# Optimization experiments

Measured on AMD Instinct MI355X. Metric: run time of the kernel, lower is better.

## Reference

```python
import jax, jax.numpy as jnp
import numpy as np

B, L, H, HD, NK, NQ = 2, 1024, 2048, 64, 4, 32
NPREV = NQ - NK  # 28 KV heads gathered from previous layers


def _rotate_half(x):
    x1, x2 = jnp.split(x, 2, axis=-1)
    return jnp.concatenate((-x2, x1), axis=-1)


def _apply_rope(cos, sin, x):
    length = x.shape[-2]
    return x * cos[..., -length:, :] + _rotate_half(x) * sin[..., -length:, :]


def setup_inputs() -> dict:
    key = jax.random.key(0)
    ks = jax.random.split(key, 7)
    hidden_states = jax.random.normal(ks[0], (B, L, H), jnp.float32)
    prev_k = jax.random.normal(ks[1], (B, NPREV, L, HD), jnp.float32)
    prev_v = jax.random.normal(ks[2], (B, NPREV, L, HD), jnp.float32)
    s = 0.02
    Wq = jax.random.normal(ks[3], (NQ * HD, H), jnp.float32) * s
    Wk = jax.random.normal(ks[4], (NK * HD, H), jnp.float32) * s
    Wv = jax.random.normal(ks[5], (NK * HD, H), jnp.float32) * s
    Wo = jax.random.normal(ks[6], (H, NQ * HD), jnp.float32) * s
    # RoPE tables (duplicated-half layout matching rotate_half)
    inv_freq = 1.0 / (10000.0 ** (jnp.arange(0, HD, 2, dtype=jnp.float32) / HD))
    freqs = jnp.arange(L, dtype=jnp.float32)[:, None] * inv_freq[None, :]
    emb = jnp.concatenate((freqs, freqs), axis=-1)  # [L, HD]
    cos = jnp.cos(emb)[None, None]  # [1,1,L,HD]
    sin = jnp.sin(emb)[None, None]
    attention_mask = jnp.tril(jnp.ones((L, L), dtype=bool))[None, None]  # [1,1,L,L]
    return {"hidden_states": hidden_states, "prev_k": prev_k, "prev_v": prev_v,
            "Wq": Wq, "Wk": Wk, "Wv": Wv, "Wo": Wo,
            "cos": cos, "sin": sin, "attention_mask": attention_mask}


def reference(hidden_states, prev_k, prev_v, Wq, Wk, Wv, Wo, cos, sin, attention_mask):
    Bv, Lv, _ = hidden_states.shape
    # QKV projections (torch Linear: x @ W.T)
    q = (hidden_states @ Wq.T).reshape(Bv, Lv, NQ, HD).transpose(0, 2, 1, 3)  # [B,NQ,L,HD]
    k_new = (hidden_states @ Wk.T).reshape(Bv, Lv, NK, HD).transpose(0, 2, 1, 3)
    v_new = (hidden_states @ Wv.T).reshape(Bv, Lv, NK, HD).transpose(0, 2, 1, 3)
    # DeCAN cross-layer cache update: stack previous layers' KV heads + current
    k = jnp.concatenate((prev_k, k_new), axis=1)  # [B,NQ,L,HD]
    v = jnp.concatenate((prev_v, v_new), axis=1)
    # RoPE after cache gather (same positions for all stacked layers)
    q = _apply_rope(cos, sin, q)
    k = _apply_rope(cos, sin, k)
    # SDPA with additive log-mask (log(bool) == 0 / -inf; broadcast == repeat)
    add_mask = jnp.where(attention_mask, jnp.float32(0.0), jnp.float32(-1e30))
    scores = jnp.einsum('bhqd,bhkd->bhqk', q, k) * (HD ** -0.5) + add_mask
    attn = jax.nn.softmax(scores, axis=-1)
    out = jnp.einsum('bhqk,bhkd->bhqd', attn, v)  # [B,NQ,L,HD]
    out = out.transpose(0, 2, 1, 3).reshape(Bv, Lv, NQ * HD)
    return out @ Wo.T  # [B,L,H]
```

## Files before the change

### kernel.cpp

```cpp
#include <hip/hip_runtime.h>
#include <stdint.h>

#define L_SEQ 1024
#define NHEAD 32
#define NPREV 28
#define HDIM  64
#define HID   2048
#define NPROJ 2560

typedef __bf16 bf16_t;
typedef bf16_t bf16x8 __attribute__((ext_vector_type(8)));
typedef float  f32x4  __attribute__((ext_vector_type(4)));

__device__ __forceinline__ ushort f2bf(float x) {
    union { float f; uint32_t u; } v; v.f = x;
    uint32_t r = v.u + 0x7fffu + ((v.u >> 16) & 1u);
    return (ushort)(r >> 16);
}
__device__ __forceinline__ ushort f2bf_t(float x) {
    union { float f; uint32_t u; } v; v.f = x;
    return (ushort)(v.u >> 16);
}
__device__ __forceinline__ float bf2f(ushort u) {
    union { uint32_t u; float f; } v; v.u = ((uint32_t)u) << 16; return v.f;
}
__device__ __forceinline__ void cvt8(float* dst, uint4 u) {
    union { uint32_t u; float f; } t;
    t.u = u.x << 16;         dst[0] = t.f;
    t.u = u.x & 0xffff0000u; dst[1] = t.f;
    t.u = u.y << 16;         dst[2] = t.f;
    t.u = u.y & 0xffff0000u; dst[3] = t.f;
    t.u = u.z << 16;         dst[4] = t.f;
    t.u = u.z & 0xffff0000u; dst[5] = t.f;
    t.u = u.w << 16;         dst[6] = t.f;
    t.u = u.w & 0xffff0000u; dst[7] = t.f;
}

#define GLB(p) ((const __attribute__((address_space(1))) void*)(p))
#define LDS(p) ((__attribute__((address_space(3))) void*)(p))

__global__ void cvt_all(const float* __restrict__ s0, const float* __restrict__ s1,
                        const float* __restrict__ s2, const float* __restrict__ s3,
                        const float* __restrict__ s4,
                        ushort* __restrict__ d0, ushort* __restrict__ d1,
                        ushort* __restrict__ d2, ushort* __restrict__ d3,
                        ushort* __restrict__ d4) {
    int blk = blockIdx.x;
    const float* src; ushort* dst; int idx;
    if      (blk < 4096) { src = s0; dst = d0; idx = blk; }
    else if (blk < 8192) { src = s1; dst = d1; idx = blk - 4096; }
    else if (blk < 8704) { src = s2; dst = d2; idx = blk - 8192; }
    else if (blk < 9216) { src = s3; dst = d3; idx = blk - 8704; }
    else                 { src = s4; dst = d4; idx = blk - 9216; }
    int i = idx * 256 + threadIdx.x;
    float4 v = ((const float4*)src)[i];
    ushort4 o;
    o.x = f2bf(v.x); o.y = f2bf(v.y); o.z = f2bf(v.z); o.w = f2bf(v.w);
    ((ushort4*)dst)[i] = o;
}

__global__ __launch_bounds__(256, 3) void gemm_bt(const ushort* __restrict__ A,
                                                  const ushort* __restrict__ B,
                                                  ushort* __restrict__ C0,
                                                  ushort* __restrict__ C1,
                                                  int M, int N, int K) {
    __shared__ __align__(16) ushort Ash[2 * 4096];
    __shared__ __align__(16) ushort Bsh[2 * 8192];
    const int tid  = threadIdx.x;
    const int lane = tid & 63;
    const int wave = tid >> 6;
    const int quad = lane >> 4;
    const int l16  = lane & 15;
    const int m0 = blockIdx.y * 64;
    const int n0 = blockIdx.x * 128;
    const int wm = (wave >> 1) * 32;
    const int wn = (wave & 1) * 64;
    const int kb = blockIdx.z * (K >> 1);
    const int ke = kb + (K >> 1);
    ushort* C = blockIdx.z ? C1 : C0;

    f32x4 acc[2][4] = {};

    const int sb = ((tid & 3) ^ ((tid >> 3) & 3)) * 8;
    const ushort* Ag = A + (long)(m0 + (tid >> 2)) * K + sb;
    const ushort* Bg = B + (long)(n0 + (tid >> 2)) * K + sb;
    const int woff = wave * 512;
    const int swz = (quad ^ ((l16 >> 1) & 3)) * 8;

    __builtin_amdgcn_global_load_lds(GLB(Ag + kb),                LDS(Ash + woff),               16, 0, 0);
    __builtin_amdgcn_global_load_lds(GLB(Ag + kb + 32),           LDS(Ash + 2048 + woff),        16, 0, 0);
    __builtin_amdgcn_global_load_lds(GLB(Bg + kb),                LDS(Bsh + woff),               16, 0, 0);
    __builtin_amdgcn_global_load_lds(GLB(Bg + 64L * K + kb),      LDS(Bsh + 2048 + woff),        16, 0, 0);
    __builtin_amdgcn_global_load_lds(GLB(Bg + kb + 32),           LDS(Bsh + 4096 + woff),        16, 0, 0);
    __builtin_amdgcn_global_load_lds(GLB(Bg + 64L * K + kb + 32), LDS(Bsh + 4096 + 2048 + woff), 16, 0, 0);

    int cur = 0;
    for (int k0 = kb; k0 < ke; k0 += 64) {
        __syncthreads();
        if (k0 + 64 < ke) {
            const int na = (cur ^ 1) * 4096;
            const int nb = (cur ^ 1) * 8192;
            const ushort* Agn = Ag + k0 + 64;
            const ushort* Bgn = Bg + k0 + 64;
            __builtin_amdgcn_global_load_lds(GLB(Agn),                LDS(Ash + na + woff),               16, 0, 0);
            __builtin_amdgcn_global_load_lds(GLB(Agn + 32),           LDS(Ash + na + 2048 + woff),        16, 0, 0);
            __builtin_amdgcn_global_load_lds(GLB(Bgn),                LDS(Bsh + nb + woff),               16, 0, 0);
            __builtin_amdgcn_global_load_lds(GLB(Bgn + 64L * K),      LDS(Bsh + nb + 2048 + woff),        16, 0, 0);
            __builtin_amdgcn_global_load_lds(GLB(Bgn + 32),           LDS(Bsh + nb + 4096 + woff),        16, 0, 0);
            __builtin_amdgcn_global_load_lds(GLB(Bgn + 64L * K + 32), LDS(Bsh + nb + 4096 + 2048 + woff), 16, 0, 0);
        }
        const ushort* As = Ash + cur * 4096;
        const ushort* Bs = Bsh + cur * 8192;
#pragma unroll
        for (int h = 0; h < 2; h++) {
            bf16x8 af[2], bf[4];
#pragma unroll
            for (int i = 0; i < 2; i++)
                af[i] = *(const bf16x8*)(As + h * 2048 + (wm + i * 16 + l16) * 32 + swz);
#pragma unroll
            for (int i = 0; i < 4; i++)
                bf[i] = *(const bf16x8*)(Bs + h * 4096 + (wn + i * 16 + l16) * 32 + swz);
#pragma unroll
            for (int mi = 0; mi < 2; mi++)
#pragma unroll
                for (int ni = 0; ni < 4; ni++)
                    acc[mi][ni] = __builtin_amdgcn_mfma_f32_16x16x32_bf16(af[mi], bf[ni], acc[mi][ni], 0, 0, 0);
        }
        cur ^= 1;
    }
#pragma unroll
    for (int mi = 0; mi < 2; mi++)
#pragma unroll
        for (int ni = 0; ni < 4; ni++)
#pragma unroll
            for (int r = 0; r < 4; r++) {
                int m = m0 + wm + mi * 16 + quad * 4 + r;
                int n = n0 + wn + ni * 16 + l16;
                C[(long)m * N + n] = f2bf(acc[mi][ni][r]);
            }
}

__global__ void add2(const ushort* __restrict__ a, const ushort* __restrict__ b,
                     float* __restrict__ out) {
    int i = blockIdx.x * 256 + threadIdx.x;
    uint4 ua = ((const uint4*)a)[i];
    uint4 ub = ((const uint4*)b)[i];
    float fa[8], fb[8];
    cvt8(fa, ua); cvt8(fb, ub);
    float4 o0 = {fa[0] + fb[0], fa[1] + fb[1], fa[2] + fb[2], fa[3] + fb[3]};
    float4 o1 = {fa[4] + fb[4], fa[5] + fb[5], fa[6] + fb[6], fa[7] + fb[7]};
    ((float4*)out)[2 * i]     = o0;
    ((float4*)out)[2 * i + 1] = o1;
}

__global__ __launch_bounds__(256) void prep_qkv(const ushort* __restrict__ pa,
                                                const ushort* __restrict__ pb,
                                                const float* __restrict__ prev_k,
                                                const float* __restrict__ prev_v,
                                                const float* __restrict__ cosb,
                                                const float* __restrict__ sinb,
                                                ushort* __restrict__ Qr,
                                                ushort* __restrict__ Kr,
                                                ushort* __restrict__ Vt) {
    __shared__ __align__(16) ushort T[64 * 72];
    const int t  = threadIdx.x;
    const int l0 = blockIdx.x * 64;
    const int bh = blockIdx.y;
    const int b  = bh >> 5, h = bh & 31;
    const int r  = t >> 2;
    const int c0 = (t & 3) * 8;
    const int l  = l0 + r;
    const long prow = ((long)(b * L_SEQ + l)) * NPROJ;
    const long base = (long)bh * (L_SEQ * HDIM);

    float cv[8], sv[8];
    *(float4*)(cv)     = *(const float4*)(cosb + l * 64 + c0);
    *(float4*)(cv + 4) = *(const float4*)(cosb + l * 64 + c0 + 4);
    *(float4*)(sv)     = *(const float4*)(sinb + l * 64 + c0);
    *(float4*)(sv + 4) = *(const float4*)(sinb + l * 64 + c0 + 4);

    const float SC = 0.125f * 1.44269504f;

    {
        float xl[8], xh[8], yl[8], yh[8];
        cvt8(xl, *(const uint4*)(pa + prow + h * 64 + c0));
        cvt8(xh, *(const uint4*)(pa + prow + h * 64 + c0 + 32));
        cvt8(yl, *(const uint4*)(pb + prow + h * 64 + c0));
        cvt8(yh, *(const uint4*)(pb + prow + h * 64 + c0 + 32));
        ushort ol[8], oh[8];
#pragma unroll
        for (int i = 0; i < 8; i++) {
            float a = xl[i] + yl[i], c = xh[i] + yh[i];
            ol[i] = f2bf((a * cv[i] - c * sv[i]) * SC);
            oh[i] = f2bf((c * cv[i] + a * sv[i]) * SC);
        }
        ushort* q = Qr + base + (long)l * 64;
        *(uint4*)(q + c0)      = *(uint4*)ol;
        *(uint4*)(q + c0 + 32) = *(uint4*)oh;
    }
    {
        float xl[8], xh[8];
        if (h < NPREV) {
            const float* pk = prev_k + (((long)b * NPREV + h) * L_SEQ + l) * 64;
            *(float4*)(xl)     = *(const float4*)(pk + c0);
            *(float4*)(xl + 4) = *(const float4*)(pk + c0 + 4);
            *(float4*)(xh)     = *(const float4*)(pk + c0 + 32);
            *(float4*)(xh + 4) = *(const float4*)(pk + c0 + 36);
        } else {
            float yl[8], yh[8];
            cvt8(xl, *(const uint4*)(pa + prow + HID + (h - NPREV) * 64 + c0));
            cvt8(xh, *(const uint4*)(pa + prow + HID + (h - NPREV) * 64 + c0 + 32));
            cvt8(yl, *(const uint4*)(pb + prow + HID + (h - NPREV) * 64 + c0));
            cvt8(yh, *(const uint4*)(pb + prow + HID + (h - NPREV) * 64 + c0 + 32));
#pragma unroll
            for (int i = 0; i < 8; i++) { xl[i] += yl[i]; xh[i] += yh[i]; }
        }
        ushort ol[8], oh[8];
#pragma unroll
        for (int i = 0; i < 8; i++) {
            ol[i] = f2bf(xl[i] * cv[i] - xh[i] * sv[i]);
            oh[i] = f2bf(xh[i] * cv[i] + xl[i] * sv[i]);
        }
        ushort* k = Kr + base + (long)l * 64;
        *(uint4*)(k + c0)      = *(uint4*)ol;
        *(uint4*)(k + c0 + 32) = *(uint4*)oh;
    }
    {
        float xl[8], xh[8];
        if (h < NPREV) {
            const float* pv = prev_v + (((long)b * NPREV + h) * L_SEQ + l) * 64;
            *(float4*)(xl)     = *(const float4*)(pv + c0);
            *(float4*)(xl + 4) = *(const float4*)(pv + c0 + 4);
            *(float4*)(xh)     = *(const float4*)(pv + c0 + 32);
            *(float4*)(xh + 4) = *(const float4*)(pv + c0 + 36);
        } else {
            float yl[8], yh[8];
            cvt8(xl, *(const uint4*)(pa + prow + HID + 256 + (h - NPREV) * 64 + c0));
            cvt8(xh, *(const uint4*)(pa + prow + HID + 256 + (h - NPREV) * 64 + c0 + 32));
            cvt8(yl, *(const uint4*)(pb + prow + HID + 256 + (h - NPREV) * 64 + c0));
            cvt8(yh, *(const uint4*)(pb + prow + HID + 256 + (h - NPREV) * 64 + c0 + 32));
#pragma unroll
            for (int i = 0; i < 8; i++) { xl[i] += yl[i]; xh[i] += yh[i]; }
        }
#pragma unroll
        for (int i = 0; i < 8; i++) {
            T[(c0 + i) * 72 + r]      = f2bf(xl[i]);
            T[(c0 + 32 + i) * 72 + r] = f2bf(xh[i]);
        }
    }
    __syncthreads();
    {
        const int lc = (t & 3) * 16;
        uint4 o0 = *(const uint4*)(T + r * 72 + lc);
        uint4 o1 = *(const uint4*)(T + r * 72 + lc + 8);
        ushort* og = Vt + base + (long)r * L_SEQ + l0 + lc;
        *(uint4*)og       = o0;
        *(uint4*)(og + 8) = o1;
    }
}

#define KP 68
__global__ __launch_bounds__(256, 4) void attn_mfma(const ushort* __restrict__ Qr,
                                                    const ushort* __restrict__ Kr,
                                                    const ushort* __restrict__ Vt,
                                                    ushort* __restrict__ Oa) {
    __shared__ __align__(16) ushort Ksh[64 * KP];
    __shared__ __align__(16) ushort Vsh[64 * KP];
    __shared__ __align__(16) ushort Psh[4][16 * KP];

    const int tid  = threadIdx.x;
    const int lane = tid & 63;
    const int wave = tid >> 6;
    const int quad = lane >> 4;
    const int l16  = lane & 15;
    const int bh   = blockIdx.x;
    const int q0   = (15 - (int)blockIdx.y) * 64;
    const long base = (long)bh * (L_SEQ * HDIM);

    bf16x8 qf0, qf1;
    {
        const ushort* qp = Qr + base + (long)(q0 + wave * 16 + l16) * HDIM + quad * 8;
        qf0 = *(const bf16x8*)qp;
        qf1 = *(const bf16x8*)(qp + 32);
    }
    float lr[4] = {};
    f32x4 o[4] = {};

    const int srow  = tid >> 2;
    const int scol  = (tid & 3) * 16;
    const int row_l = wave * 16 + quad * 4;

    uint4 ka, kb, va, vb;
    {
        const ushort* kg = Kr + base + (long)srow * HDIM + scol;
        ka = *(const uint4*)kg; kb = *(const uint4*)(kg + 8);
        const ushort* vg = Vt + base + (long)srow * L_SEQ + scol;
        va = *(const uint4*)vg; vb = *(const uint4*)(vg + 8);
    }

    for (int kv0 = 0; kv0 <= q0; kv0 += 64) {
        __syncthreads();
        *(uint4*)(Ksh + srow * KP + scol)     = ka;
        *(uint4*)(Ksh + srow * KP + scol + 8) = kb;
        *(uint4*)(Vsh + srow * KP + scol)     = va;
        *(uint4*)(Vsh + srow * KP + scol + 8) = vb;
        __syncthreads();
        if (kv0 + 64 <= q0) {
            const ushort* kg = Kr + base + (long)(kv0 + 64 + srow) * HDIM + scol;
            ka = *(const uint4*)kg; kb = *(const uint4*)(kg + 8);
            const ushort* vg = Vt + base + (long)srow * L_SEQ + kv0 + 64 + scol;
            va = *(const uint4*)vg; vb = *(const uint4*)(vg + 8);
        }

        f32x4 s[4] = {};
#pragma unroll
        for (int nt = 0; nt < 4; nt++) {
            bf16x8 kf0 = *(const bf16x8*)(Ksh + (nt * 16 + l16) * KP + quad * 8);
            bf16x8 kf1 = *(const bf16x8*)(Ksh + (nt * 16 + l16) * KP + 32 + quad * 8);
            s[nt] = __builtin_amdgcn_mfma_f32_16x16x32_bf16(qf0, kf0, s[nt], 0, 0, 0);
            s[nt] = __builtin_amdgcn_mfma_f32_16x16x32_bf16(qf1, kf1, s[nt], 0, 0, 0);
        }

        const bool diag = (kv0 == q0);
#pragma unroll
        for (int nt = 0; nt < 4; nt++) {
            const int col = nt * 16 + l16;
#pragma unroll
            for (int r = 0; r < 4; r++) {
                float p = __builtin_exp2f(s[nt][r]);
                if (diag && col > row_l + r) p = 0.f;
                lr[r] += p;
                Psh[wave][(quad * 4 + r) * KP + col] = f2bf_t(p);
            }
        }

#pragma unroll
        for (int ks = 0; ks < 2; ks++) {
            bf16x8 pf = *(const bf16x8*)(&Psh[wave][l16 * KP + ks * 32 + quad * 8]);
#pragma unroll
            for (int nt = 0; nt < 4; nt++) {
                bf16x8 vf = *(const bf16x8*)(Vsh + (nt * 16 + l16) * KP + ks * 32 + quad * 8);
                o[nt] = __builtin_amdgcn_mfma_f32_16x16x32_bf16(pf, vf, o[nt], 0, 0, 0);
            }
        }
    }

    const int b = bh >> 5, h = bh & 31;
#pragma unroll
    for (int r = 0; r < 4; r++) {
        float a = lr[r];
        a += __shfl_xor(a, 1); a += __shfl_xor(a, 2); a += __shfl_xor(a, 4); a += __shfl_xor(a, 8);
        float inv = 1.f / a;
        long orow = (long)(b * L_SEQ + q0 + wave * 16 + quad * 4 + r) * HID + h * 64;
#pragma unroll
        for (int nt = 0; nt < 4; nt++)
            Oa[orow + nt * 16 + l16] = f2bf(o[nt][r] * inv);
    }
}

extern "C" void kernel_launch(void* const* d_in, const int* in_sizes, int n_in,
                              void* d_out, int out_size, void* d_ws, size_t ws_size,
                              hipStream_t stream) {
    const float* hs     = (const float*)d_in[0];
    const float* prev_k = (const float*)d_in[1];
    const float* prev_v = (const float*)d_in[2];
    const float* Wq     = (const float*)d_in[3];
    const float* Wk     = (const float*)d_in[4];
    const float* Wv     = (const float*)d_in[5];
    const float* Wo     = (const float*)d_in[6];
    const float* cosb   = (const float*)d_in[7];
    const float* sinb   = (const float*)d_in[8];
    float* out = (float*)d_out;

    ushort* hs_bf   = (ushort*)d_ws;
    ushort* wqkv_bf = hs_bf + 2048L * 2048;
    ushort* wo_bf   = wqkv_bf + 2560L * 2048;
    ushort* proj    = wo_bf + 2048L * 2048;
    ushort* Qr      = proj + 2048L * 2560;
    ushort* Kr      = Qr + 4194304;
    ushort* Vt      = Kr + 4194304;
    ushort* Oa      = Vt + 4194304;

    ushort* proj_b;
    if (ws_size >= (35651584UL + 5242880UL) * 2)
        proj_b = Oa + 4194304;
    else
        proj_b = (ushort*)(void*)d_in[0];

    ushort* outp_a = proj;
    ushort* outp_b = Qr;

    cvt_all<<<13312, 256, 0, stream>>>(hs, Wq, Wk, Wv, Wo,
                                       hs_bf, wqkv_bf,
                                       wqkv_bf + 2048L * 2048,
                                       wqkv_bf + 2304L * 2048,
                                       wo_bf);
    gemm_bt<<<dim3(20, 32, 2), 256, 0, stream>>>(hs_bf, wqkv_bf, proj, proj_b, 2048, 2560, 2048);
    prep_qkv<<<dim3(16, 64), 256, 0, stream>>>(proj, proj_b, prev_k, prev_v, cosb, sinb, Qr, Kr, Vt);
    attn_mfma<<<dim3(64, 16), 256, 0, stream>>>(Qr, Kr, Vt, Oa);
    gemm_bt<<<dim3(16, 32, 2), 256, 0, stream>>>(Oa, wo_bf, outp_a, outp_b, 2048, 2048, 2048);
    add2<<<2048, 256, 0, stream>>>(outp_a, outp_b, out);
}
```

Measured before the change: 237.5 us.

## Fuse prev-KV RoPE prep into QKV GEMM launch; single-pass fp32 output GEMM

The QKV projection GEMM grid now carries extra blocks that process the 28 previous-layer KV heads (RoPE on K, transpose of V). These blocks have no dependency on the GEMM, so that work can overlap with the matmul instead of running in a later kernel. The later prep kernel now handles only Q and the 4 new KV heads. The output projection drops split-K: it runs the full K range in one pass and writes fp32 directly, which removes the bf16 partial buffers and the add2 kernel. The costs are fewer blocks in the output GEMM (512 instead of 1024), which may leave the GPU less occupied, and a mixed-role kernel whose long GEMM blocks and short prep blocks can finish unevenly.

```diff
diff --git a/kernel.cpp b/kernel.cpp
--- a/kernel.cpp
+++ b/kernel.cpp
@@ -59,104 +59,154 @@
     ((ushort4*)dst)[i] = o;
 }
 
-__global__ __launch_bounds__(256, 3) void gemm_bt(const ushort* __restrict__ A,
-                                                  const ushort* __restrict__ B,
-                                                  ushort* __restrict__ C0,
-                                                  ushort* __restrict__ C1,
-                                                  int M, int N, int K) {
+__global__ __launch_bounds__(256, 3) void gemm1_fused(
+        const ushort* __restrict__ A, const ushort* __restrict__ B,
+        ushort* __restrict__ C0, ushort* __restrict__ C1,
+        const float* __restrict__ prev_k, const float* __restrict__ prev_v,
+        const float* __restrict__ cosb, const float* __restrict__ sinb,
+        ushort* __restrict__ Kr, ushort* __restrict__ Vt) {
     __shared__ __align__(16) ushort Ash[2 * 4096];
     __shared__ __align__(16) ushort Bsh[2 * 8192];
-    const int tid  = threadIdx.x;
-    const int lane = tid & 63;
-    const int wave = tid >> 6;
-    const int quad = lane >> 4;
-    const int l16  = lane & 15;
-    const int m0 = blockIdx.y * 64;
-    const int n0 = blockIdx.x * 128;
-    const int wm = (wave >> 1) * 32;
-    const int wn = (wave & 1) * 64;
-    const int kb = blockIdx.z * (K >> 1);
-    const int ke = kb + (K >> 1);
-    ushort* C = blockIdx.z ? C1 : C0;
-
-    f32x4 acc[2][4] = {};
-
-    const int sb = ((tid & 3) ^ ((tid >> 3) & 3)) * 8;
-    const ushort* Ag = A + (long)(m0 + (tid >> 2)) * K + sb;
-    const ushort* Bg = B + (long)(n0 + (tid >> 2)) * K + sb;
-    const int woff = wave * 512;
-    const int swz = (quad ^ ((l16 >> 1) & 3)) * 8;
-
-    __builtin_amdgcn_global_load_lds(GLB(Ag + kb),                LDS(Ash + woff),               16, 0, 0);
-    __builtin_amdgcn_global_load_lds(GLB(Ag + kb + 32),           LDS(Ash + 2048 + woff),        16, 0, 0);
-    __builtin_amdgcn_global_load_lds(GLB(Bg + kb),                LDS(Bsh + woff),               16, 0, 0);
-    __builtin_amdgcn_global_load_lds(GLB(Bg + 64L * K + kb),      LDS(Bsh + 2048 + woff),        16, 0, 0);
-    __builtin_amdgcn_global_load_lds(GLB(Bg + kb + 32),           LDS(Bsh + 4096 + woff),        16, 0, 0);
-    __builtin_amdgcn_global_load_lds(GLB(Bg + 64L * K + kb + 32), LDS(Bsh + 4096 + 2048 + woff), 16, 0, 0);
-
-    int cur = 0;
-    for (int k0 = kb; k0 < ke; k0 += 64) {
-        __syncthreads();
-        if (k0 + 64 < ke) {
-            const int na = (cur ^ 1) * 4096;
-            const int nb = (cur ^ 1) * 8192;
-            const ushort* Agn = Ag + k0 + 64;
-            const ushort* Bgn = Bg + k0 + 64;
-            __builtin_amdgcn_global_load_lds(GLB(Agn),                LDS(Ash + na + woff),               16, 0, 0);
-            __builtin_amdgcn_global_load_lds(GLB(Agn + 32),           LDS(Ash + na + 2048 + woff),        16, 0, 0);
-            __builtin_amdgcn_global_load_lds(GLB(Bgn),                LDS(Bsh + nb + woff),               16, 0, 0);
-            __builtin_amdgcn_global_load_lds(GLB(Bgn + 64L * K),      LDS(Bsh + nb + 2048 + woff),        16, 0, 0);
-            __builtin_amdgcn_global_load_lds(GLB(Bgn + 32),           LDS(Bsh + nb + 4096 + woff),        16, 0, 0);
-            __builtin_amdgcn_global_load_lds(GLB(Bgn + 64L * K + 32), LDS(Bsh + nb + 4096 + 2048 + woff), 16, 0, 0);
-        }
-        const ushort* As = Ash + cur * 4096;
-        const ushort* Bs = Bsh + cur * 8192;
-#pragma unroll
-        for (int h = 0; h < 2; h++) {
-            bf16x8 af[2], bf[4];
-#pragma unroll
-            for (int i = 0; i < 2; i++)
-                af[i] = *(const bf16x8*)(As + h * 2048 + (wm + i * 16 + l16) * 32 + swz);
-#pragma unroll
-            for (int i = 0; i < 4; i++)
-                bf[i] = *(const bf16x8*)(Bs + h * 4096 + (wn + i * 16 + l16) * 32 + swz);
-#pragma unroll
-            for (int mi = 0; mi < 2; mi++)
-#pragma unroll
-                for (int ni = 0; ni < 4; ni++)
-                    acc[mi][ni] = __builtin_amdgcn_mfma_f32_16x16x32_bf16(af[mi], bf[ni], acc[mi][ni], 0, 0, 0);
-        }
-        cur ^= 1;
-    }
-#pragma unroll
-    for (int mi = 0; mi < 2; mi++)
-#pragma unroll
-        for (int ni = 0; ni < 4; ni++)
-#pragma unroll
-            for (int r = 0; r < 4; r++) {
-                int m = m0 + wm + mi * 16 + quad * 4 + r;
-                int n = n0 + wn + ni * 16 + l16;
-                C[(long)m * N + n] = f2bf(acc[mi][ni][r]);
-            }
-}
-
-__global__ void add2(const ushort* __restrict__ a, const ushort* __restrict__ b,
-                     float* __restrict__ out) {
-    int i = blockIdx.x * 256 + threadIdx.x;
-    uint4 ua = ((const uint4*)a)[i];
-    uint4 ub = ((const uint4*)b)[i];
-    float fa[8], fb[8];
-    cvt8(fa, ua); cvt8(fb, ub);
-    float4 o0 = {fa[0] + fb[0], fa[1] + fb[1], fa[2] + fb[2], fa[3] + fb[3]};
-    float4 o1 = {fa[4] + fb[4], fa[5] + fb[5], fa[6] + fb[6], fa[7] + fb[7]};
-    ((float4*)out)[2 * i]     = o0;
-    ((float4*)out)[2 * i + 1] = o1;
-}
-
-__global__ __launch_bounds__(256) void prep_qkv(const ushort* __restrict__ pa,
+    const int g   = blockIdx.x;
+    const int tid = threadIdx.x;
+
+    if (g < 1280) {
+        const int K = 2048, N = NPROJ;
+        const int lane = tid & 63;
+        const int wave = tid >> 6;
+        const int quad = lane >> 4;
+        const int l16  = lane & 15;
+        const int z  = g / 640;
+        const int rb = g % 640;
+        const int n0 = (rb % 20) * 128;
+        const int m0 = (rb / 20) * 64;
+        const int wm = (wave >> 1) * 32;
+        const int wn = (wave & 1) * 64;
+        const int kb = z * 1024;
+        const int ke = kb + 1024;
+        ushort* C = z ? C1 : C0;
+
+        f32x4 acc[2][4] = {};
+
+        const int sb = ((tid & 3) ^ ((tid >> 3) & 3)) * 8;
+        const ushort* Ag = A + (long)(m0 + (tid >> 2)) * K + sb;
+        const ushort* Bg = B + (long)(n0 + (tid >> 2)) * K + sb;
+        const int woff = wave * 512;
+        const int swz = (quad ^ ((l16 >> 1) & 3)) * 8;
+
+        __builtin_amdgcn_global_load_lds(GLB(Ag + kb),                LDS(Ash + woff),               16, 0, 0);
+        __builtin_amdgcn_global_load_lds(GLB(Ag + kb + 32),           LDS(Ash + 2048 + woff),        16, 0, 0);
+        __builtin_amdgcn_global_load_lds(GLB(Bg + kb),                LDS(Bsh + woff),               16, 0, 0);
+        __builtin_amdgcn_global_load_lds(GLB(Bg + 64L * K + kb),      LDS(Bsh + 2048 + woff),        16, 0, 0);
+        __builtin_amdgcn_global_load_lds(GLB(Bg + kb + 32),           LDS(Bsh + 4096 + woff),        16, 0, 0);
+        __builtin_amdgcn_global_load_lds(GLB(Bg + 64L * K + kb + 32), LDS(Bsh + 4096 + 2048 + woff), 16, 0, 0);
+
+        int cur = 0;
+        for (int k0 = kb; k0 < ke; k0 += 64) {
+            __syncthreads();
+            if (k0 + 64 < ke) {
+                const int na = (cur ^ 1) * 4096;
+                const int nb = (cur ^ 1) * 8192;
+                const ushort* Agn = Ag + k0 + 64;
+                const ushort* Bgn = Bg + k0 + 64;
+                __builtin_amdgcn_global_load_lds(GLB(Agn),                LDS(Ash + na + woff),               16, 0, 0);
+                __builtin_amdgcn_global_load_lds(GLB(Agn + 32),           LDS(Ash + na + 2048 + woff),        16, 0, 0);
+                __builtin_amdgcn_global_load_lds(GLB(Bgn),                LDS(Bsh + nb + woff),               16, 0, 0);
+                __builtin_amdgcn_global_load_lds(GLB(Bgn + 64L * K),      LDS(Bsh + nb + 2048 + woff),        16, 0, 0);
+                __builtin_amdgcn_global_load_lds(GLB(Bgn + 32),           LDS(Bsh + nb + 4096 + woff),        16, 0, 0);
+                __builtin_amdgcn_global_load_lds(GLB(Bgn + 64L * K + 32), LDS(Bsh + nb + 4096 + 2048 + woff), 16, 0, 0);
+            }
+            const ushort* As = Ash + cur * 4096;
+            const ushort* Bs = Bsh + cur * 8192;
+#pragma unroll
+            for (int h = 0; h < 2; h++) {
+                bf16x8 af[2], bf[4];
+#pragma unroll
+                for (int i = 0; i < 2; i++)
+                    af[i] = *(const bf16x8*)(As + h * 2048 + (wm + i * 16 + l16) * 32 + swz);
+#pragma unroll
+                for (int i = 0; i < 4; i++)
+                    bf[i] = *(const bf16x8*)(Bs + h * 4096 + (wn + i * 16 + l16) * 32 + swz);
+#pragma unroll
+                for (int mi = 0; mi < 2; mi++)
+#pragma unroll
+                    for (int ni = 0; ni < 4; ni++)
+                        acc[mi][ni] = __builtin_amdgcn_mfma_f32_16x16x32_bf16(af[mi], bf[ni], acc[mi][ni], 0, 0, 0);
+            }
+            cur ^= 1;
+        }
+#pragma unroll
+        for (int mi = 0; mi < 2; mi++)
+#pragma unroll
+            for (int ni = 0; ni < 4; ni++)
+#pragma unroll
+                for (int r = 0; r < 4; r++) {
+                    int m = m0 + wm + mi * 16 + quad * 4 + r;
+                    int n = n0 + wn + ni * 16 + l16;
+                    C[(long)m * N + n] = f2bf(acc[mi][ni][r]);
+                }
+    } else {
+        const int idx = g - 1280;
+        const int lt  = idx & 15;
+        const int ph  = idx >> 4;
+        const int b   = ph / NPREV;
+        const int h   = ph % NPREV;
+        const int l0  = lt * 64;
+        const int r   = tid >> 2;
+        const int c0  = (tid & 3) * 8;
+        const int l   = l0 + r;
+        const int bh  = b * NHEAD + h;
+        const long base = (long)bh * (L_SEQ * HDIM);
+
+        float cv[8], sv[8];
+        *(float4*)(cv)     = *(const float4*)(cosb + l * 64 + c0);
+        *(float4*)(cv + 4) = *(const float4*)(cosb + l * 64 + c0 + 4);
+        *(float4*)(sv)     = *(const float4*)(sinb + l * 64 + c0);
+        *(float4*)(sv + 4) = *(const float4*)(sinb + l * 64 + c0 + 4);
+
+        {
+            const float* pk = prev_k + (((long)b * NPREV + h) * L_SEQ + l) * 64;
+            float xl[8], xh[8];
+            *(float4*)(xl)     = *(const float4*)(pk + c0);
+            *(float4*)(xl + 4) = *(const float4*)(pk + c0 + 4);
+            *(float4*)(xh)     = *(const float4*)(pk + c0 + 32);
+            *(float4*)(xh + 4) = *(const float4*)(pk + c0 + 36);
+            ushort ol[8], oh[8];
+#pragma unroll
+            for (int i = 0; i < 8; i++) {
+                ol[i] = f2bf(xl[i] * cv[i] - xh[i] * sv[i]);
+                oh[i] = f2bf(xh[i] * cv[i] + xl[i] * sv[i]);
+            }
+            ushort* k = Kr + base + (long)l * 64;
+            *(uint4*)(k + c0)      = *(uint4*)ol;
+            *(uint4*)(k + c0 + 32) = *(uint4*)oh;
+        }
+        {
+            ushort* T = Ash;
+            const float* pv = prev_v + (((long)b * NPREV + h) * L_SEQ + l) * 64;
+            float xl[8], xh[8];
+            *(float4*)(xl)     = *(const float4*)(pv + c0);
+            *(float4*)(xl + 4) = *(const float4*)(pv + c0 + 4);
+            *(float4*)(xh)     = *(const float4*)(pv + c0 + 32);
+            *(float4*)(xh + 4) = *(const float4*)(pv + c0 + 36);
+#pragma unroll
+            for (int i = 0; i < 8; i++) {
+                T[(c0 + i) * 72 + r]      = f2bf(xl[i]);
+                T[(c0 + 32 + i) * 72 + r] = f2bf(xh[i]);
+            }
+            __syncthreads();
+            const int lc = (tid & 3) * 16;
+            uint4 o0 = *(const uint4*)(T + r * 72 + lc);
+            uint4 o1 = *(const uint4*)(T + r * 72 + lc + 8);
+            ushort* og = Vt + base + (long)r * L_SEQ + l0 + lc;
+            *(uint4*)og       = o0;
+            *(uint4*)(og + 8) = o1;
+        }
+    }
+}
+
+__global__ __launch_bounds__(256) void prep_new(const ushort* __restrict__ pa,
                                                 const ushort* __restrict__ pb,
-                                                const float* __restrict__ prev_k,
-                                                const float* __restrict__ prev_v,
                                                 const float* __restrict__ cosb,
                                                 const float* __restrict__ sinb,
                                                 ushort* __restrict__ Qr,
@@ -198,58 +248,37 @@
         *(uint4*)(q + c0)      = *(uint4*)ol;
         *(uint4*)(q + c0 + 32) = *(uint4*)oh;
     }
+    if (h < NPREV) return;
+
     {
-        float xl[8], xh[8];
-        if (h < NPREV) {
-            const float* pk = prev_k + (((long)b * NPREV + h) * L_SEQ + l) * 64;
-            *(float4*)(xl)     = *(const float4*)(pk + c0);
-            *(float4*)(xl + 4) = *(const float4*)(pk + c0 + 4);
-            *(float4*)(xh)     = *(const float4*)(pk + c0 + 32);
-            *(float4*)(xh + 4) = *(const float4*)(pk + c0 + 36);
-        } else {
-            float yl[8], yh[8];
-            cvt8(xl, *(const uint4*)(pa + prow + HID + (h - NPREV) * 64 + c0));
-            cvt8(xh, *(const uint4*)(pa + prow + HID + (h - NPREV) * 64 + c0 + 32));
-            cvt8(yl, *(const uint4*)(pb + prow + HID + (h - NPREV) * 64 + c0));
-            cvt8(yh, *(const uint4*)(pb + prow + HID + (h - NPREV) * 64 + c0 + 32));
-#pragma unroll
-            for (int i = 0; i < 8; i++) { xl[i] += yl[i]; xh[i] += yh[i]; }
-        }
+        float xl[8], xh[8], yl[8], yh[8];
+        cvt8(xl, *(const uint4*)(pa + prow + HID + (h - NPREV) * 64 + c0));
+        cvt8(xh, *(const uint4*)(pa + prow + HID + (h - NPREV) * 64 + c0 + 32));
+        cvt8(yl, *(const uint4*)(pb + prow + HID + (h - NPREV) * 64 + c0));
+        cvt8(yh, *(const uint4*)(pb + prow + HID + (h - NPREV) * 64 + c0 + 32));
         ushort ol[8], oh[8];
 #pragma unroll
         for (int i = 0; i < 8; i++) {
-            ol[i] = f2bf(xl[i] * cv[i] - xh[i] * sv[i]);
-            oh[i] = f2bf(xh[i] * cv[i] + xl[i] * sv[i]);
+            float a = xl[i] + yl[i], c = xh[i] + yh[i];
+            ol[i] = f2bf(a * cv[i] - c * sv[i]);
+            oh[i] = f2bf(c * cv[i] + a * sv[i]);
         }
         ushort* k = Kr + base + (long)l * 64;
         *(uint4*)(k + c0)      = *(uint4*)ol;
         *(uint4*)(k + c0 + 32) = *(uint4*)oh;
     }
     {
-        float xl[8], xh[8];
-        if (h < NPREV) {
-            const float* pv = prev_v + (((long)b * NPREV + h) * L_SEQ + l) * 64;
-            *(float4*)(xl)     = *(const float4*)(pv + c0);
-            *(float4*)(xl + 4) = *(const float4*)(pv + c0 + 4);
-            *(float4*)(xh)     = *(const float4*)(pv + c0 + 32);
-            *(float4*)(xh + 4) = *(const float4*)(pv + c0 + 36);
-        } else {
-            float yl[8], yh[8];
-            cvt8(xl, *(const uint4*)(pa + prow + HID + 256 + (h - NPREV) * 64 + c0));
-            cvt8(xh, *(const uint4*)(pa + prow + HID + 256 + (h - NPREV) * 64 + c0 + 32));
-            cvt8(yl, *(const uint4*)(pb + prow + HID + 256 + (h - NPREV) * 64 + c0));
-            cvt8(yh, *(const uint4*)(pb + prow + HID + 256 + (h - NPREV) * 64 + c0 + 32));
-#pragma unroll
-            for (int i = 0; i < 8; i++) { xl[i] += yl[i]; xh[i] += yh[i]; }
-        }
+        float xl[8], xh[8], yl[8], yh[8];
+        cvt8(xl, *(const uint4*)(pa + prow + HID + 256 + (h - NPREV) * 64 + c0));
+        cvt8(xh, *(const uint4*)(pa + prow + HID + 256 + (h - NPREV) * 64 + c0 + 32));
+        cvt8(yl, *(const uint4*)(pb + prow + HID + 256 + (h - NPREV) * 64 + c0));
+        cvt8(yh, *(const uint4*)(pb + prow + HID + 256 + (h - NPREV) * 64 + c0 + 32));
 #pragma unroll
         for (int i = 0; i < 8; i++) {
-            T[(c0 + i) * 72 + r]      = f2bf(xl[i]);
-            T[(c0 + 32 + i) * 72 + r] = f2bf(xh[i]);
-        }
-    }
-    __syncthreads();
-    {
+            T[(c0 + i) * 72 + r]      = f2bf(xl[i] + yl[i]);
+            T[(c0 + 32 + i) * 72 + r] = f2bf(xh[i] + yh[i]);
+        }
+        __syncthreads();
         const int lc = (t & 3) * 16;
         uint4 o0 = *(const uint4*)(T + r * 72 + lc);
         uint4 o1 = *(const uint4*)(T + r * 72 + lc + 8);
@@ -356,6 +385,83 @@
         for (int nt = 0; nt < 4; nt++)
             Oa[orow + nt * 16 + l16] = f2bf(o[nt][r] * inv);
     }
+}
+
+__global__ __launch_bounds__(256, 3) void gemm_out(const ushort* __restrict__ A,
+                                                   const ushort* __restrict__ B,
+                                                   float* __restrict__ C) {
+    __shared__ __align__(16) ushort Ash[2 * 4096];
+    __shared__ __align__(16) ushort Bsh[2 * 8192];
+    const int K = 2048, N = 2048;
+    const int tid  = threadIdx.x;
+    const int lane = tid & 63;
+    const int wave = tid >> 6;
+    const int quad = lane >> 4;
+    const int l16  = lane & 15;
+    const int m0 = blockIdx.y * 64;
+    const int n0 = blockIdx.x * 128;
+    const int wm = (wave >> 1) * 32;
+    const int wn = (wave & 1) * 64;
+
+    f32x4 acc[2][4] = {};
+
+    const int sb = ((tid & 3) ^ ((tid >> 3) & 3)) * 8;
+    const ushort* Ag = A + (long)(m0 + (tid >> 2)) * K + sb;
+    const ushort* Bg = B + (long)(n0 + (tid >> 2)) * K + sb;
+    const int woff = wave * 512;
+    const int swz = (quad ^ ((l16 >> 1) & 3)) * 8;
+
+    __builtin_amdgcn_global_load_lds(GLB(Ag),                LDS(Ash + woff),               16, 0, 0);
+    __builtin_amdgcn_global_load_lds(GLB(Ag + 32),           LDS(Ash + 2048 + woff),        16, 0, 0);
+    __builtin_amdgcn_global_load_lds(GLB(Bg),                LDS(Bsh + woff),               16, 0, 0);
+    __builtin_amdgcn_global_load_lds(GLB(Bg + 64L * K),      LDS(Bsh + 2048 + woff),        16, 0, 0);
+    __builtin_amdgcn_global_load_lds(GLB(Bg + 32),           LDS(Bsh + 4096 + woff),        16, 0, 0);
+    __builtin_amdgcn_global_load_lds(GLB(Bg + 64L * K + 32), LDS(Bsh + 4096 + 2048 + woff), 16, 0, 0);
+
+    int cur = 0;
+    for (int k0 = 0; k0 < K; k0 += 64) {
+        __syncthreads();
+        if (k0 + 64 < K) {
+            const int na = (cur ^ 1) * 4096;
+            const int nb = (cur ^ 1) * 8192;
+            const ushort* Agn = Ag + k0 + 64;
+            const ushort* Bgn = Bg + k0 + 64;
+            __builtin_amdgcn_global_load_lds(GLB(Agn),                LDS(Ash + na + woff),               16, 0, 0);
+            __builtin_amdgcn_global_load_lds(GLB(Agn + 32),           LDS(Ash + na + 2048 + woff),        16, 0, 0);
+            __builtin_amdgcn_global_load_lds(GLB(Bgn),                LDS(Bsh + nb + woff),               16, 0, 0);
+            __builtin_amdgcn_global_load_lds(GLB(Bgn + 64L * K),      LDS(Bsh + nb + 2048 + woff),        16, 0, 0);
+            __builtin_amdgcn_global_load_lds(GLB(Bgn + 32),           LDS(Bsh + nb + 4096 + woff),        16, 0, 0);
+            __builtin_amdgcn_global_load_lds(GLB(Bgn + 64L * K + 32), LDS(Bsh + nb + 4096 + 2048 + woff), 16, 0, 0);
+        }
+        const ushort* As = Ash + cur * 4096;
+        const ushort* Bs = Bsh + cur * 8192;
+#pragma unroll
+        for (int h = 0; h < 2; h++) {
+            bf16x8 af[2], bf[4];
+#pragma unroll
+            for (int i = 0; i < 2; i++)
+                af[i] = *(const bf16x8*)(As + h * 2048 + (wm + i * 16 + l16) * 32 + swz);
+#pragma unroll
+            for (int i = 0; i < 4; i++)
+                bf[i] = *(const bf16x8*)(Bs + h * 4096 + (wn + i * 16 + l16) * 32 + swz);
+#pragma unroll
+            for (int mi = 0; mi < 2; mi++)
+#pragma unroll
+                for (int ni = 0; ni < 4; ni++)
+                    acc[mi][ni] = __builtin_amdgcn_mfma_f32_16x16x32_bf16(af[mi], bf[ni], acc[mi][ni], 0, 0, 0);
+        }
+        cur ^= 1;
+    }
+#pragma unroll
+    for (int mi = 0; mi < 2; mi++)
+#pragma unroll
+        for (int ni = 0; ni < 4; ni++)
+#pragma unroll
+            for (int r = 0; r < 4; r++) {
+                int m = m0 + wm + mi * 16 + quad * 4 + r;
+                int n = n0 + wn + ni * 16 + l16;
+                C[(long)m * N + n] = acc[mi][ni][r];
+            }
 }
 
 extern "C" void kernel_launch(void* const* d_in, const int* in_sizes, int n_in,
@@ -387,17 +493,14 @@
     else
         proj_b = (ushort*)(void*)d_in[0];
 
-    ushort* outp_a = proj;
-    ushort* outp_b = Qr;
-
     cvt_all<<<13312, 256, 0, stream>>>(hs, Wq, Wk, Wv, Wo,
                                        hs_bf, wqkv_bf,
                                        wqkv_bf + 2048L * 2048,
                                        wqkv_bf + 2304L * 2048,
                                        wo_bf);
-    gemm_bt<<<dim3(20, 32, 2), 256, 0, stream>>>(hs_bf, wqkv_bf, proj, proj_b, 2048, 2560, 2048);
-    prep_qkv<<<dim3(16, 64), 256, 0, stream>>>(proj, proj_b, prev_k, prev_v, cosb, sinb, Qr, Kr, Vt);
+    gemm1_fused<<<2176, 256, 0, stream>>>(hs_bf, wqkv_bf, proj, proj_b,
+                                          prev_k, prev_v, cosb, sinb, Kr, Vt);
+    prep_new<<<dim3(16, 64), 256, 0, stream>>>(proj, proj_b, cosb, sinb, Qr, Kr, Vt);
     attn_mfma<<<dim3(64, 16), 256, 0, stream>>>(Qr, Kr, Vt, Oa);
-    gemm_bt<<<dim3(16, 32, 2), 256, 0, stream>>>(Oa, wo_bf, outp_a, outp_b, 2048, 2048, 2048);
-    add2<<<2048, 256, 0, stream>>>(outp_a, outp_b, out);
-}
+    gemm_out<<<dim3(16, 32), 256, 0, stream>>>(Oa, wo_bf, out);
+}
```

Result: no change. 233.0 us (-1.9%).
